# Performance work log

Hardware: AMD Instinct MI355X
Metric: run time of the kernel (lower is better)

## Reference

```python
import jax, jax.numpy as jnp
from jax import lax
import numpy as np

D = 512        # d_model
F = 128        # raw feature dim
MS = 1024      # logic (service) nodes
NP_ = 16384    # physical nodes
EL = 4096      # logic edges
EP = 131072    # phys edges
SRC = 0        # source_node_idx
NEG = -1e9


def _gnn(feats, edge_index, Win, Wout, N):
    row, col = edge_index
    h = jax.nn.relu(feats @ Win)                                  # [N, D]
    agg = jax.ops.segment_sum(h[row], col, num_segments=N)        # [N, D]
    return jax.nn.relu((h + agg) @ Wout)


def _bfs_hop(edge_index, N, src, iters=16):
    # BFS hop distance from src (bounded Bellman-Ford relaxation)
    row, col = edge_index
    big = jnp.int32(N)
    dist = jnp.full((N,), big, jnp.int32).at[src].set(0)
    def body(_, d):
        cand = jnp.minimum(d[row] + 1, big)
        upd = jax.ops.segment_min(cand, col, num_segments=N)
        return jnp.minimum(d, upd)
    return lax.fori_loop(0, iters, body, dist)


def _forward(logic_feats, phys_feats, Ws_in, Ws_out, Wp_in, Wp_out,
             sA1, sA2, pA1, pA2, Wq, Wk, Wc1, bc1, wc2,
             logic_edge_index, phys_edge_index, actions, static_mask, topo_order):
    Np = phys_feats.shape[0]
    cloud = Np - 1                                                # cloud_node_idx = -1
    h_s = _gnn(logic_feats, logic_edge_index, Ws_in, Ws_out, logic_feats.shape[0])
    h_p = _gnn(phys_feats, phys_edge_index, Wp_in, Wp_out, Np)
    # task-specific residual adapters
    h_s = h_s + jax.nn.relu(h_s @ sA1) @ sA2
    h_p = h_p + jax.nn.relu(h_p @ pA1) @ pA2
    metric = _bfs_hop(phys_edge_index, Np, SRC)                   # [Np] int32
    q_all = (h_s @ Wq) / jnp.sqrt(jnp.float32(D))                 # [Ms, D]
    K = h_p @ Wk                                                  # [Np, D]
    acts = actions.astype(jnp.int32)

    def step(state, i):
        visited, last, logp_sum, ent_sum, switches, relax = state
        base = static_mask[i]                                     # [Np] bool
        # cloud_sticky branch
        sticky = jnp.zeros_like(base).at[cloud].set(base[cloud])
        # forbid_return (allow_stay keeps `last`)
        forbid = visited.at[last].set(False)
        allowed_n = base & (~forbid) & (metric >= metric[last])   # metric_non_decreasing
        allowed = jnp.where(last == cloud, sticky, allowed_n)
        any_a = allowed.any()
        # relaxation fallback: stay -> cloud -> base
        fb_stay = jnp.zeros_like(base).at[last].set(True)
        fb_cloud = jnp.zeros_like(base).at[cloud].set(True)
        fallback = jnp.where(base[last], fb_stay, jnp.where(base[cloud], fb_cloud, base))
        allowed = jnp.where(any_a, allowed, fallback)
        # actor: masked categorical over physical nodes
        logits = K @ q_all[i]                                     # [Np]
        logp_all = jax.nn.log_softmax(jnp.where(allowed, logits, NEG))
        p = jnp.exp(logp_all)
        ent = -jnp.sum(p * logp_all)
        a = acts[i]
        ne = a != last
        visited = visited.at[last].set(visited[last] | ne)
        last = jnp.where(ne, a, last)
        return (visited, last, logp_sum + logp_all[a], ent_sum + ent,
                switches + ne.astype(jnp.int32), relax + (~any_a).astype(jnp.int32)), None

    init = (jnp.zeros((Np,), bool), jnp.int32(SRC),
            jnp.float32(0.0), jnp.float32(0.0), jnp.int32(0), jnp.int32(0))
    (visited, last, logp_sum, ent_sum, switches, relax), _ = lax.scan(
        step, init, topo_order.astype(jnp.int32))
    # value head
    pooled = jnp.concatenate([h_s.mean(0), h_p.mean(0)])          # [2D]
    value = jax.nn.relu(pooled @ Wc1 + bc1) @ wc2                 # scalar
    return jnp.stack([logp_sum, ent_sum, value])


def setup_inputs() -> dict:
    key = jax.random.key(0)
    ks = jax.random.split(key, 20)
    s = 0.05
    def w(k, shape):
        return jax.random.normal(k, shape, jnp.float32) * s
    return {
        "logic_edge_index": jax.random.randint(ks[0], (2, EL), 0, MS, jnp.int32),
        "logic_feats": jax.random.normal(ks[1], (MS, F), jnp.float32),
        "phys_edge_index": jax.random.randint(ks[2], (2, EP), 0, NP_, jnp.int32),
        "phys_feats": jax.random.normal(ks[3], (NP_, F), jnp.float32),
        "actions": jax.random.randint(ks[4], (MS,), 0, NP_, jnp.int32),
        "static_mask": jnp.ones((MS, NP_), bool),
        "topo_order": jnp.arange(MS, dtype=jnp.int32),
        "Ws_in": w(ks[5], (F, D)), "Ws_out": w(ks[6], (D, D)),
        "Wp_in": w(ks[7], (F, D)), "Wp_out": w(ks[8], (D, D)),
        "sA1": w(ks[9], (D, D)), "sA2": w(ks[10], (D, D)),
        "pA1": w(ks[11], (D, D)), "pA2": w(ks[12], (D, D)),
        "Wq": w(ks[13], (D, D)), "Wk": w(ks[14], (D, D)),
        "Wc1": w(ks[15], (2 * D, D)),
        "bc1": jnp.zeros((D,), jnp.float32),
        "wc2": w(ks[16], (D,)),
    }


def reference(logic_edge_index, logic_feats, phys_edge_index, phys_feats,
              actions, static_mask, topo_order,
              Ws_in, Ws_out, Wp_in, Wp_out, sA1, sA2, pA1, pA2,
              Wq, Wk, Wc1, bc1, wc2):
    return _forward(logic_feats, phys_feats, Ws_in, Ws_out, Wp_in, Wp_out,
                    sA1, sA2, pA1, pA2, Wq, Wk, Wc1, bc1, wc2,
                    logic_edge_index, phys_edge_index, actions, static_mask, topo_order)
```

## Files before the change

### kernel.cpp

```cpp
#include <hip/hip_runtime.h>
#include <cstdint>
#include <cstddef>

typedef __bf16 bf16_t;
typedef uint8_t u8;
typedef float f32x4 __attribute__((ext_vector_type(4)));

#define NEGV (-1e9f)

#define GLDS(gp, lp) __builtin_amdgcn_global_load_lds( \
    (const __attribute__((address_space(1))) void*)(gp), \
    (__attribute__((address_space(3))) void*)(lp), 16, 0, 0)

template<int SEL>
__device__ inline float fp8decw(uint32_t w) { return __builtin_amdgcn_cvt_f32_fp8((int)w, SEL); }
__device__ inline float fp8dec(u8 b) { return __builtin_amdgcn_cvt_f32_fp8((int)b, 0); }
__device__ inline u8 f2fp8(float x) {
    return (u8)(__builtin_amdgcn_cvt_pk_fp8_f32(x, x, 0, false) & 0xFF);
}

__device__ inline void bfs_level_work(const int* __restrict__ offR, const int* __restrict__ ecol,
                                      int* __restrict__ dist, int lev, int blk, int tid) {
    int j = blk * 256 + tid;
    if (dist[j] != lev) return;
    int e0 = offR[j], e1 = offR[j + 1];
    for (int e = e0; e < e1; ++e) {
        int v = ecol[e];
        if (dist[v] == 16384) dist[v] = lev + 1;
    }
}

struct PrepArgs {
    const float* w512src[8]; u8* w512dst[8];
    const float* w128src[2]; u8* w128dst[2];
    const float* logicF; const float* physF;
    u8* featsSb; u8* featsPb;
    const int* mask; uint32_t* bits;
    int* cntC; int* cntR; int* cntL; int* firstL; int* dist;
    float* pooled; float* hacc;
};

__global__ __launch_bounds__(256)
void k_prep(PrepArgs p) {
    __shared__ float tb[64][65];
    const int b = blockIdx.x, tid = threadIdx.x;
    if (b < 544) {
        const float* src; u8* dst; int K, tile;
        if (b < 512) { src = p.w512src[b >> 6]; dst = p.w512dst[b >> 6]; K = 512; tile = b & 63; }
        else { int bb = b - 512; src = p.w128src[bb >> 4]; dst = p.w128dst[bb >> 4]; K = 128; tile = bb & 15; }
        const int N = 512;
        int kt = tile >> 3, tc = tile & 7;
        int cx = tid & 63, ry = tid >> 6;
#pragma unroll
        for (int q = 0; q < 16; ++q) {
            int r = q * 4 + ry;
            tb[r][cx] = src[(size_t)(kt * 64 + r) * N + tc * 64 + cx];
        }
        __syncthreads();
#pragma unroll
        for (int q = 0; q < 16; ++q) {
            int r2 = q * 4 + ry;
            dst[(size_t)(tc * 64 + r2) * K + kt * 64 + cx] = f2fp8(tb[cx][r2]);
        }
    } else if (b < 672) {
        size_t e0 = (size_t)(b - 544) * 1024 + tid * 4;
        float4 v = *(const float4*)(p.logicF + e0);
        int pk = __builtin_amdgcn_cvt_pk_fp8_f32(v.x, v.y, 0, false);
        pk = __builtin_amdgcn_cvt_pk_fp8_f32(v.z, v.w, pk, true);
        *(uint32_t*)(p.featsSb + e0) = (uint32_t)pk;
    } else if (b < 2720) {
        size_t e0 = (size_t)(b - 672) * 1024 + tid * 4;
        float4 v = *(const float4*)(p.physF + e0);
        int pk = __builtin_amdgcn_cvt_pk_fp8_f32(v.x, v.y, 0, false);
        pk = __builtin_amdgcn_cvt_pk_fp8_f32(v.z, v.w, pk, true);
        *(uint32_t*)(p.featsPb + e0) = (uint32_t)pk;
    } else if (b < 2784) {
        int gid = (b - 2720) * 256 + tid;
        p.cntC[gid] = 0; p.cntR[gid] = 0; p.firstL[gid] = 0x7fffffff;
        p.dist[gid] = (gid == 0) ? 0 : 16384;
        if (gid < 1024) { p.cntL[gid] = 0; p.pooled[gid] = 0.0f; }
        if (gid < 512) p.hacc[gid] = 0.0f;
    } else {
        size_t w = (size_t)(b - 2784) * 256 + tid;
        const int4* q4 = (const int4*)(p.mask + w * 32);
        uint32_t bb = 0;
#pragma unroll
        for (int q = 0; q < 8; ++q) {
            int4 v = q4[q];
            bb |= (v.x != 0 ? 1u : 0u) << (q * 4);
            bb |= (v.y != 0 ? 1u : 0u) << (q * 4 + 1);
            bb |= (v.z != 0 ? 1u : 0u) << (q * 4 + 2);
            bb |= (v.w != 0 ? 1u : 0u) << (q * 4 + 3);
        }
        p.bits[w] = bb;
    }
}

__global__ void k_hist3(const int* __restrict__ rowP, const int* __restrict__ colP,
                        const int* __restrict__ rowL, const int* __restrict__ colL,
                        int* cntC, int* cntR, int* cntL, int EP, int EL,
                        const int* __restrict__ topo, const int* __restrict__ acts,
                        int* __restrict__ lastArr, int* __restrict__ firstL) {
    int b = blockIdx.x;
    if (b < 1040) {
        int e = b * 256 + threadIdx.x;
        if (e < EP) atomicAdd(&cntC[colP[e]], 1);
        else if (e < 2 * EP) atomicAdd(&cntR[rowP[e - EP]], 1);
        else if (e < 2 * EP + EL) atomicAdd(&cntL[colL[e - 2 * EP]], 1);
    } else {
        int s = (b - 1040) * 256 + threadIdx.x;
        int last = (s == 0) ? 0 : acts[topo[s - 1]];
        lastArr[s] = last;
        int a = acts[topo[s]];
        if (a != last) atomicMin(&firstL[last], s);
    }
}

__global__ __launch_bounds__(256)
void k_scan3(int* cntC, int* offC, int* curC,
             int* cntR, int* offR, int* curR,
             int* cntL, int* offL, int* curL) {
    __shared__ int ss[256];
    const int tid = threadIdx.x;
    if (blockIdx.x < 2) {
        int* cnt; int* off; int* cur;
        if (blockIdx.x == 0) { cnt = cntC; off = offC; cur = curC; }
        else                 { cnt = cntR; off = offR; cur = curR; }
        int4 v[16];
        const int4* pv = (const int4*)(cnt + tid * 64);
#pragma unroll
        for (int i = 0; i < 16; ++i) v[i] = pv[i];
        int s = 0;
#pragma unroll
        for (int i = 0; i < 16; ++i) s += v[i].x + v[i].y + v[i].z + v[i].w;
        ss[tid] = s; __syncthreads();
        for (int d = 1; d < 256; d <<= 1) {
            int t = (tid >= d) ? ss[tid - d] : 0;
            __syncthreads(); ss[tid] += t; __syncthreads();
        }
        int run = (tid == 0) ? 0 : ss[tid - 1];
        int4* po = (int4*)(off + tid * 64);
        int4* pc = (int4*)(cur + tid * 64);
#pragma unroll
        for (int i = 0; i < 16; ++i) {
            int4 o;
            o.x = run; run += v[i].x;
            o.y = run; run += v[i].y;
            o.z = run; run += v[i].z;
            o.w = run; run += v[i].w;
            po[i] = o; pc[i] = o;
        }
        if (tid == 255) off[16384] = run;
    } else {
        int4 v = *(const int4*)(cntL + tid * 4);
        int s = v.x + v.y + v.z + v.w;
        ss[tid] = s; __syncthreads();
        for (int d = 1; d < 256; d <<= 1) {
            int t = (tid >= d) ? ss[tid - d] : 0;
            __syncthreads(); ss[tid] += t; __syncthreads();
        }
        int run = (tid == 0) ? 0 : ss[tid - 1];
        int4 o;
        o.x = run; run += v.x;
        o.y = run; run += v.y;
        o.z = run; run += v.z;
        o.w = run; run += v.w;
        *(int4*)(offL + tid * 4) = o;
        *(int4*)(curL + tid * 4) = o;
        if (tid == 255) offL[1024] = run;
    }
}

__global__ void k_scatter3(const int* __restrict__ rowP, const int* __restrict__ colP,
                           const int* __restrict__ rowL, const int* __restrict__ colL,
                           int* curC, int* curR, int* curL,
                           int* erowCP, int* ecolRP, int* erowL, int EP, int EL) {
    int e = blockIdx.x * 256 + threadIdx.x;
    if (e < EP) {
        int c = colP[e]; int q = atomicAdd(&curC[c], 1); erowCP[q] = rowP[e];
    } else if (e < 2 * EP) {
        int e2 = e - EP;
        int c = rowP[e2]; int q = atomicAdd(&curR[c], 1); ecolRP[q] = colP[e2];
    } else if (e < 2 * EP + EL) {
        int e3 = e - 2 * EP;
        int c = colL[e3]; int q = atomicAdd(&curL[c], 1); erowL[q] = rowL[e3];
    }
}

__global__ __launch_bounds__(256)
void k_bfs_level(const int* __restrict__ offR, const int* __restrict__ ecol,
                 int* __restrict__ dist, int lev) {
    bfs_level_work(offR, ecol, dist, lev, blockIdx.x, threadIdx.x);
}

__global__ __launch_bounds__(256)
void k_fmpack(const int* __restrict__ firstL, const int* __restrict__ dist, int* __restrict__ fm) {
    int j = blockIdx.x * 256 + threadIdx.x;
    int fl = firstL[j]; if (fl > 0xFFFF) fl = 0xFFFF;
    fm[j] = (fl << 16) | dist[j];
}

struct GemmDesc { const u8* A; const u8* B; const u8* Cin; void* O;
                  int N; int K; float scale; int relu; int obf; };
struct GemmPair { GemmDesc d0; GemmDesc d1; int split; int gx; int nwg;
                  const int* offR; const int* ecol; int* dist; int bfsLev; };

__global__ __launch_bounds__(256)
void gemm_mfma(GemmPair args) {
    __shared__ u8 As[2][128 * 64];
    __shared__ u8 Bs[2][128 * 64];
    const int tid = threadIdx.x;
    int f = blockIdx.x;
    if (f < 64) {
        bfs_level_work(args.offR, args.ecol, args.dist, args.bfsLev, f, tid);
        return;
    }
    f -= 64;
    const int cpx = args.nwg >> 3;
    const int vfl = (f & 7) * cpx + (f >> 3);
    const int vbx = vfl % args.gx;
    const int vby = vfl / args.gx;
    const int inSet1 = (vby >= args.split);
    const GemmDesc g = inSet1 ? args.d1 : args.d0;
    const int my = vby - (inSet1 ? args.split : 0);
    const int m0 = my * 128, n0 = vbx * 128;
    const int wave = tid >> 6, lane = tid & 63;
    const int wm = (wave >> 1) * 64, wn = (wave & 1) * 64;
    const int lr = lane & 15, lkq = lane >> 4;
    const int K = g.K;
    const int srr = wave * 16 + (lane >> 2);
    const int scb = (((lane & 3) ^ ((lane >> 2) & 3)) << 4);
    const u8* Abase = g.A + (size_t)(m0 + srr) * K + scb;
    const u8* Bbase = g.B + (size_t)(n0 + srr) * K + scb;
    const size_t rstep = (size_t)64 * K;
    f32x4 acc[4][4] = {};

    auto stage = [&](int q, int k0) {
        GLDS(Abase + k0,         &As[q][(wave * 16) * 64]);
        GLDS(Abase + k0 + rstep, &As[q][(64 + wave * 16) * 64]);
        GLDS(Bbase + k0,         &Bs[q][(wave * 16) * 64]);
        GLDS(Bbase + k0 + rstep, &Bs[q][(64 + wave * 16) * 64]);
    };

    stage(0, 0);
    asm volatile("s_waitcnt vmcnt(0)" ::: "memory");
    __syncthreads();
    const int nt = K >> 6;
    for (int t = 0; t < nt; ++t) {
        int cur = t & 1;
        if (t + 1 < nt) stage(cur ^ 1, (t + 1) << 6);
#pragma unroll
        for (int kh = 0; kh < 2; ++kh) {
            long af[4], bf[4];
#pragma unroll
            for (int mi = 0; mi < 4; ++mi) {
                int r = wm + mi * 16 + lr;
                int pb = r * 64 + ((kh * 32 + lkq * 8) ^ ((r & 3) << 4));
                af[mi] = *(const long*)&As[cur][pb];
            }
#pragma unroll
            for (int ni = 0; ni < 4; ++ni) {
                int r = wn + ni * 16 + lr;
                int pb = r * 64 + ((kh * 32 + lkq * 8) ^ ((r & 3) << 4));
                bf[ni] = *(const long*)&Bs[cur][pb];
            }
#pragma unroll
            for (int mi = 0; mi < 4; ++mi)
#pragma unroll
                for (int ni = 0; ni < 4; ++ni)
                    acc[mi][ni] = __builtin_amdgcn_mfma_f32_16x16x32_fp8_fp8(af[mi], bf[ni], acc[mi][ni], 0, 0, 0);
        }
        asm volatile("s_waitcnt vmcnt(0)" ::: "memory");
        __syncthreads();
    }
    const int rb = m0 + wm + (lane >> 4) * 4;
    const int cb = n0 + wn + lr;
#pragma unroll
    for (int mi = 0; mi < 4; ++mi)
#pragma unroll
        for (int ni = 0; ni < 4; ++ni)
#pragma unroll
            for (int r = 0; r < 4; ++r) {
                int row = rb + mi * 16 + r;
                int col = cb + ni * 16;
                size_t idx = (size_t)row * g.N + col;
                float v = acc[mi][ni][r] * g.scale;
                if (g.Cin) v += fp8dec(g.Cin[idx]);
                if (g.relu) v = fmaxf(v, 0.0f);
                if (g.obf) ((bf16_t*)g.O)[idx] = (bf16_t)v;
                else       ((u8*)g.O)[idx] = f2fp8(v);
            }
}

__global__ __launch_bounds__(256)
void k_spmm2(const u8* __restrict__ HL, const int* __restrict__ offL, const int* __restrict__ erowL, u8* __restrict__ XL,
             const u8* __restrict__ HP, const int* __restrict__ offP, const int* __restrict__ erowP, u8* __restrict__ XP,
             const int* __restrict__ offR, const int* __restrict__ ecol, int* __restrict__ dist, int bfsLev) {
    int b = blockIdx.x;
    if (b < 64) { bfs_level_work(offR, ecol, dist, bfsLev, b, threadIdx.x); return; }
    b -= 64;
    const u8* H; const int* off; const int* erow; u8* X; int c;
    int wib = threadIdx.x >> 6, lane = threadIdx.x & 63;
    if (b < 256) { H = HL; off = offL; erow = erowL; X = XL; c = b * 4 + wib; }
    else { b -= 256; H = HP; off = offP; erow = erowP; X = XP; c = b * 4 + wib; }
    int d0 = lane * 8;
    float acc[8] = {0,0,0,0,0,0,0,0};
    int e0 = off[c], e1 = off[c + 1];
    for (int e = e0; e < e1; ++e) {
        int r = erow[e];
        uint2 w = *(const uint2*)(H + (size_t)r * 512 + d0);
        acc[0] += fp8decw<0>(w.x);
        acc[1] += fp8decw<1>(w.x);
        acc[2] += fp8decw<2>(w.x);
        acc[3] += fp8decw<3>(w.x);
        acc[4] += fp8decw<0>(w.y);
        acc[5] += fp8decw<1>(w.y);
        acc[6] += fp8decw<2>(w.y);
        acc[7] += fp8decw<3>(w.y);
    }
    uint2 ow = *(const uint2*)(H + (size_t)c * 512 + d0);
    float o0 = fp8decw<0>(ow.x) + acc[0];
    float o1 = fp8decw<1>(ow.x) + acc[1];
    float o2 = fp8decw<2>(ow.x) + acc[2];
    float o3 = fp8decw<3>(ow.x) + acc[3];
    float o4 = fp8decw<0>(ow.y) + acc[4];
    float o5 = fp8decw<1>(ow.y) + acc[5];
    float o6 = fp8decw<2>(ow.y) + acc[6];
    float o7 = fp8decw<3>(ow.y) + acc[7];
    int lo = __builtin_amdgcn_cvt_pk_fp8_f32(o0, o1, 0, false);
    lo = __builtin_amdgcn_cvt_pk_fp8_f32(o2, o3, lo, true);
    int hi = __builtin_amdgcn_cvt_pk_fp8_f32(o4, o5, 0, false);
    hi = __builtin_amdgcn_cvt_pk_fp8_f32(o6, o7, hi, true);
    uint2 res; res.x = (uint32_t)lo; res.y = (uint32_t)hi;
    *(uint2*)(X + (size_t)c * 512 + d0) = res;
}

__global__ __launch_bounds__(256)
void k_scan2(const bf16_t* __restrict__ S, const uint32_t* __restrict__ bits,
             const int* __restrict__ fm, const int* __restrict__ topo,
             const int* __restrict__ acts, const int* __restrict__ lastA,
             float* __restrict__ slogp, float* __restrict__ sent) {
    typedef bf16_t bf16x8 __attribute__((ext_vector_type(8)));
    const int NPn = 16384, cloud = NPn - 1;
    __shared__ float msh[256], zsh[256], wsh[256];
    __shared__ int ash[256];
    const int s = blockIdx.x, tid = threadIdx.x;
    const int i = topo[s], a = acts[i], last = lastA[s];
    const bf16_t* Srow = S + (size_t)i * NPn;
    const uint32_t* brow = bits + (size_t)i * 512;
    const int ml = fm[last] & 0xFFFF;
    const int baseCloud = (brow[511] >> 31) & 1;
    const int lic = (last == cloud);
    if (lic && baseCloud) {
        if (tid == 0) {
            float M = (float)Srow[cloud];
            slogp[s] = (a == cloud) ? 0.0f : (NEGV - M);
            sent[s] = 0.0f;
        }
        return;
    }
    float m = -3.4e38f, Z = 0.0f, W = 0.0f;
    int any = 0;
    if (!lic) {
        for (int c = 0; c < 8; ++c) {
            int j0 = c * 2048 + tid * 8;
            bf16x8 sv = *(const bf16x8*)(Srow + j0);
            uint32_t b8 = (brow[j0 >> 5] >> (j0 & 24)) & 0xFFu;
            int4 f0 = *(const int4*)(fm + j0);
            int4 f1 = *(const int4*)(fm + j0 + 4);
            int fj[8] = {f0.x, f0.y, f0.z, f0.w, f1.x, f1.y, f1.z, f1.w};
#pragma unroll
            for (int q = 0; q < 8; ++q) {
                int j = j0 + q;
                bool alw = ((b8 >> q) & 1) && ((fj[q] & 0xFFFF) >= ml)
                           && (j == last || (((unsigned)fj[q]) >> 16) >= (unsigned)s);
                if (alw) {
                    any = 1;
                    float l = (float)sv[q];
                    if (l > m) {
                        float d = m - l, ce = expf(d);
                        W = ce * (W + d * Z);
                        Z = ce * Z + 1.0f;
                        m = l;
                    } else {
                        float t = l - m, e = expf(t);
                        Z += e; W += t * e;
                    }
                }
            }
        }
    }
    msh[tid] = m; zsh[tid] = Z; wsh[tid] = W; ash[tid] = any;
    __syncthreads();
    for (int st = 128; st > 0; st >>= 1) {
        if (tid < st) {
            float m1 = msh[tid], Z1 = zsh[tid], W1 = wsh[tid];
            float m2 = msh[tid + st], Z2 = zsh[tid + st], W2 = wsh[tid + st];
            float M2 = fmaxf(m1, m2);
            float e1 = expf(m1 - M2), e2 = expf(m2 - M2);
            zsh[tid] = e1 * Z1 + e2 * Z2;
            wsh[tid] = e1 * (W1 + (m1 - M2) * Z1) + e2 * (W2 + (m2 - M2) * Z2);
            msh[tid] = M2;
            ash[tid] |= ash[tid + st];
        }
        __syncthreads();
    }
    if (tid != 0) return;
    if (ash[0]) {
        float M = msh[0], Zt = zsh[0], Wt = wsh[0];
        float logZ = logf(Zt);
        int fa = fm[a];
        bool alwa = ((brow[a >> 5] >> (a & 31)) & 1) && ((fa & 0xFFFF) >= ml)
                    && (a == last || (((unsigned)fa) >> 16) >= (unsigned)s);
        float la = alwa ? (float)Srow[a] : NEGV;
        slogp[s] = la - M - logZ;
        sent[s] = logZ - Wt / Zt;
        return;
    }
    int baseLast = (brow[last >> 5] >> (last & 31)) & 1;
    if (baseLast) { float M = (float)Srow[last]; slogp[s] = (a == last) ? 0.0f : (NEGV - M); sent[s] = 0.0f; return; }
    if (baseCloud) { float M = (float)Srow[cloud]; slogp[s] = (a == cloud) ? 0.0f : (NEGV - M); sent[s] = 0.0f; return; }
    float mm = -3.4e38f, ZZ = 0.0f, WW = 0.0f;
    for (int j = 0; j < NPn; ++j) {
        if ((brow[j >> 5] >> (j & 31)) & 1) {
            float l = (float)Srow[j];
            if (l > mm) { float d = mm - l, ce = expf(d); WW = ce * (WW + d * ZZ); ZZ = ce * ZZ + 1.0f; mm = l; }
            else { float t = l - mm, e = expf(t); ZZ += e; WW += t * e; }
        }
    }
    if (ZZ == 0.0f) { slogp[s] = -logf((float)NPn); sent[s] = logf((float)NPn); return; }
    float logZ = logf(ZZ);
    int ba = (brow[a >> 5] >> (a & 31)) & 1;
    float la = ba ? (float)Srow[a] : NEGV;
    slogp[s] = la - mm - logZ;
    sent[s] = logZ - WW / ZZ;
}

__global__ __launch_bounds__(256)
void k_pool2(const u8* __restrict__ HL, const u8* __restrict__ HP, float* __restrict__ pooled,
             const int* __restrict__ offR, const int* __restrict__ ecol, int* __restrict__ dist, int bfsLev) {
    int b = blockIdx.x, tid = threadIdx.x;
    if (b < 64) { bfs_level_work(offR, ecol, dist, bfsLev, b, tid); return; }
    b -= 64;
    const u8* H; float* dst; int R, bb, ng; float inv;
    if (b < 16) { H = HL; dst = pooled; R = 1024; inv = 1.0f / 1024.0f; bb = b; ng = 16; }
    else { H = HP; dst = pooled + 512; R = 16384; inv = 1.0f / 16384.0f; bb = b - 16; ng = 128; }
    int c0 = tid * 2;
    float a0 = 0, a1 = 0;
    for (int r = bb; r < R; r += ng) {
        uint32_t w = *(const unsigned short*)(H + (size_t)r * 512 + c0);
        a0 += fp8decw<0>(w);
        a1 += fp8decw<1>(w);
    }
    atomicAdd(&dst[c0], a0 * inv);
    atomicAdd(&dst[c0 + 1], a1 * inv);
}

__global__ __launch_bounds__(256)
void k_vpart(const float* __restrict__ pooled, const float* __restrict__ Wc1, float* __restrict__ hacc) {
    __shared__ float pk[128];
    int b = blockIdx.x, tid = threadIdx.x;
    int k0 = b * 128;
    if (tid < 128) pk[tid] = pooled[k0 + tid];
    __syncthreads();
    float a0 = 0, a1 = 0;
    for (int kk = 0; kk < 128; ++kk) {
        float pv = pk[kk];
        const float* wr = Wc1 + (size_t)(k0 + kk) * 512;
        a0 += pv * wr[tid];
        a1 += pv * wr[tid + 256];
    }
    atomicAdd(&hacc[tid], a0);
    atomicAdd(&hacc[tid + 256], a1);
}

__global__ __launch_bounds__(256)
void k_epilogue(const float* __restrict__ slogp, const float* __restrict__ sent,
                const float* __restrict__ hacc, const float* __restrict__ bc1,
                const float* __restrict__ wc2, float* __restrict__ out) {
    __shared__ float s1[256], s2[256], s3[256];
    int tid = threadIdx.x;
    float a = 0, b = 0;
    for (int k = tid; k < 1024; k += 256) { a += slogp[k]; b += sent[k]; }
    float v = fmaxf(hacc[tid] + bc1[tid], 0.0f) * wc2[tid]
            + fmaxf(hacc[tid + 256] + bc1[tid + 256], 0.0f) * wc2[tid + 256];
    s1[tid] = a; s2[tid] = b; s3[tid] = v;
    __syncthreads();
    for (int st = 128; st > 0; st >>= 1) {
        if (tid < st) { s1[tid] += s1[tid + st]; s2[tid] += s2[tid + st]; s3[tid] += s3[tid + st]; }
        __syncthreads();
    }
    if (tid == 0) { out[0] = s1[0]; out[1] = s2[0]; out[2] = s3[0]; }
}

extern "C" void kernel_launch(void* const* d_in, const int* in_sizes, int n_in,
                              void* d_out, int out_size, void* d_ws, size_t ws_size,
                              hipStream_t stream) {
    (void)n_in; (void)out_size; (void)ws_size; (void)in_sizes;
    const int MS = 1024, NP = 16384, EL = 4096, EP = 131072, D = 512;

    const int* logicE = (const int*)d_in[0];
    const float* logicF = (const float*)d_in[1];
    const int* physE = (const int*)d_in[2];
    const float* physF = (const float*)d_in[3];
    const int* acts = (const int*)d_in[4];
    const int* mask = (const int*)d_in[5];
    const int* topo = (const int*)d_in[6];
    const float* Ws_in = (const float*)d_in[7];
    const float* Ws_out = (const float*)d_in[8];
    const float* Wp_in = (const float*)d_in[9];
    const float* Wp_out = (const float*)d_in[10];
    const float* sA1 = (const float*)d_in[11];
    const float* sA2 = (const float*)d_in[12];
    const float* pA1 = (const float*)d_in[13];
    const float* pA2 = (const float*)d_in[14];
    const float* Wq = (const float*)d_in[15];
    const float* Wk = (const float*)d_in[16];
    const float* Wc1 = (const float*)d_in[17];
    const float* bc1 = (const float*)d_in[18];
    const float* wc2 = (const float*)d_in[19];
    float* out = (float*)d_out;

    char* wsb = (char*)d_ws;
    size_t off = 0;
    auto alloc = [&](size_t bytes) -> void* {
        off = (off + 255) & ~(size_t)255;
        void* p = wsb + off; off += bytes; return p;
    };

    bf16_t* S_bf  = (bf16_t*)alloc((size_t)MS * NP * 2);
    u8* PB0     = (u8*)alloc((size_t)NP * D);
    u8* PB1     = (u8*)alloc((size_t)NP * D);
    u8* PB2     = (u8*)alloc((size_t)NP * D);
    u8* LB0     = (u8*)alloc((size_t)MS * D);
    u8* LB1     = (u8*)alloc((size_t)MS * D);
    u8* LB2     = (u8*)alloc((size_t)MS * D);
    u8* featsSb = (u8*)alloc((size_t)MS * 128);
    u8* featsPb = (u8*)alloc((size_t)NP * 128);
    u8* WsinT   = (u8*)alloc(512 * 128);
    u8* WpinT   = (u8*)alloc(512 * 128);
    u8* WsoutT  = (u8*)alloc(512 * 512);
    u8* sA1T    = (u8*)alloc(512 * 512);
    u8* sA2T    = (u8*)alloc(512 * 512);
    u8* WqT     = (u8*)alloc(512 * 512);
    u8* WpoutT  = (u8*)alloc(512 * 512);
    u8* pA1T    = (u8*)alloc(512 * 512);
    u8* pA2T    = (u8*)alloc(512 * 512);
    u8* WkT     = (u8*)alloc(512 * 512);
    uint32_t* bits = (uint32_t*)alloc((size_t)MS * NP / 8);
    int* cntC  = (int*)alloc(NP * 4);
    int* offC  = (int*)alloc((NP + 1) * 4);
    int* curC  = (int*)alloc(NP * 4);
    int* cntR  = (int*)alloc(NP * 4);
    int* offR  = (int*)alloc((NP + 1) * 4);
    int* curR  = (int*)alloc(NP * 4);
    int* cntL  = (int*)alloc(MS * 4);
    int* offL  = (int*)alloc((MS + 1) * 4);
    int* curL  = (int*)alloc(MS * 4);
    int* erowCP = (int*)alloc(EP * 4);
    int* ecolRP = (int*)alloc(EP * 4);
    int* erowL  = (int*)alloc(EL * 4);
    int* firstL = (int*)alloc(NP * 4);
    int* lastA  = (int*)alloc(MS * 4);
    int* dist   = (int*)alloc(NP * 4);
    int* fm     = (int*)alloc(NP * 4);
    float* slogp = (float*)alloc(MS * 4);
    float* sentb = (float*)alloc(MS * 4);
    float* pooled = (float*)alloc(1024 * 4);
    float* hacc   = (float*)alloc(512 * 4);

    const int* rowP = physE;  const int* colP = physE + EP;
    const int* rowL = logicE; const int* colL = logicE + EL;

    {
        PrepArgs p;
        const float* s512[8] = {Ws_out, sA1, sA2, Wq, Wp_out, pA1, pA2, Wk};
        u8* d512[8] = {WsoutT, sA1T, sA2T, WqT, WpoutT, pA1T, pA2T, WkT};
        for (int q = 0; q < 8; ++q) { p.w512src[q] = s512[q]; p.w512dst[q] = d512[q]; }
        p.w128src[0] = Ws_in; p.w128dst[0] = WsinT;
        p.w128src[1] = Wp_in; p.w128dst[1] = WpinT;
        p.logicF = logicF; p.physF = physF; p.featsSb = featsSb; p.featsPb = featsPb;
        p.mask = mask; p.bits = bits;
        p.cntC = cntC; p.cntR = cntR; p.cntL = cntL; p.firstL = firstL; p.dist = dist;
        p.pooled = pooled; p.hacc = hacc;
        hipLaunchKernelGGL(k_prep, dim3(4832), dim3(256), 0, stream, p);
    }
    hipLaunchKernelGGL(k_hist3, dim3(1044), dim3(256), 0, stream,
                       rowP, colP, rowL, colL, cntC, cntR, cntL, EP, EL,
                       topo, acts, lastA, firstL);
    hipLaunchKernelGGL(k_scan3, dim3(3), dim3(256), 0, stream,
                       cntC, offC, curC, cntR, offR, curR, cntL, offL, curL);
    hipLaunchKernelGGL(k_scatter3, dim3((2 * EP + EL) / 256), dim3(256), 0, stream,
                       rowP, colP, rowL, colL, curC, curR, curL, erowCP, ecolRP, erowL, EP, EL);
    for (int lev = 0; lev < 7; ++lev)
        hipLaunchKernelGGL(k_bfs_level, dim3(64), dim3(256), 0, stream, offR, ecolRP, dist, lev);

    auto gemm2 = [&](const u8* A0, const u8* B0, const u8* C0, void* O0, float sc0,
                     const u8* A1, const u8* B1, const u8* C1, void* O1, float sc1,
                     int K, int relu, int bfsLev) {
        GemmPair gp;
        gp.d0 = {A0, B0, C0, O0, 512, K, sc0, relu, 0};
        gp.d1 = {A1, B1, C1, O1, 512, K, sc1, relu, 0};
        gp.split = 8; gp.gx = 4; gp.nwg = 544;
        gp.offR = offR; gp.ecol = ecolRP; gp.dist = dist; gp.bfsLev = bfsLev;
        hipLaunchKernelGGL(gemm_mfma, dim3(64 + 544), dim3(256), 0, stream, gp);
    };

    gemm2(featsSb, WsinT, nullptr, LB0, 1.0f, featsPb, WpinT, nullptr, PB0, 1.0f, 128, 1, 7);
    hipLaunchKernelGGL(k_spmm2, dim3(64 + 256 + 4096), dim3(256), 0, stream,
                       LB0, offL, erowL, LB1, PB0, offC, erowCP, PB1,
                       offR, ecolRP, dist, 8);
    gemm2(LB1, WsoutT, nullptr, LB0, 1.0f, PB1, WpoutT, nullptr, PB0, 1.0f, 512, 1, 9);
    gemm2(LB0, sA1T, nullptr, LB1, 1.0f, PB0, pA1T, nullptr, PB1, 1.0f, 512, 1, 10);
    gemm2(LB1, sA2T, LB0, LB2, 1.0f, PB1, pA2T, PB0, PB2, 1.0f, 512, 0, 11);
    hipLaunchKernelGGL(k_pool2, dim3(64 + 144), dim3(256), 0, stream, LB2, PB2, pooled,
                       offR, ecolRP, dist, 12);
    gemm2(LB2, WqT, nullptr, LB1, 0.044194173824159216f, PB2, WkT, nullptr, PB1, 1.0f, 512, 0, 13);
    {
        GemmPair gp;
        gp.d0 = {LB1, PB1, nullptr, S_bf, NP, 512, 1.0f, 0, 1};
        gp.d1 = gp.d0;
        gp.split = 1000; gp.gx = 128; gp.nwg = 1024;
        gp.offR = offR; gp.ecol = ecolRP; gp.dist = dist; gp.bfsLev = 14;
        hipLaunchKernelGGL(gemm_mfma, dim3(64 + 1024), dim3(256), 0, stream, gp);
    }
    hipLaunchKernelGGL(k_bfs_level, dim3(64), dim3(256), 0, stream, offR, ecolRP, dist, 15);
    hipLaunchKernelGGL(k_fmpack, dim3(64), dim3(256), 0, stream, firstL, dist, fm);
    hipLaunchKernelGGL(k_scan2, dim3(MS), dim3(256), 0, stream,
                       S_bf, bits, fm, topo, acts, lastA, slogp, sentb);
    hipLaunchKernelGGL(k_vpart, dim3(8), dim3(256), 0, stream, pooled, Wc1, hacc);
    hipLaunchKernelGGL(k_epilogue, dim3(1), dim3(256), 0, stream, slogp, sentb, hacc, bc1, wc2, out);
}
```

Baseline: 337.3 us.

## Store score matrix as fp8 and drop fmpack kernel by reading dist/firstL directly

The final score GEMM now writes the 1024x16384 logits in fp8 instead of bf16. This halves the write traffic and the read traffic for the scan kernel. The separate fmpack launch is removed, and the scan instead reads dist and firstL arrays directly, which trades one launch for extra loads per element. The risk is lower logit precision, which affects the log-prob and entropy values.

```diff
diff --git a/kernel.cpp b/kernel.cpp
--- a/kernel.cpp
+++ b/kernel.cpp
@@ -191,13 +191,6 @@
 void k_bfs_level(const int* __restrict__ offR, const int* __restrict__ ecol,
                  int* __restrict__ dist, int lev) {
     bfs_level_work(offR, ecol, dist, lev, blockIdx.x, threadIdx.x);
-}
-
-__global__ __launch_bounds__(256)
-void k_fmpack(const int* __restrict__ firstL, const int* __restrict__ dist, int* __restrict__ fm) {
-    int j = blockIdx.x * 256 + threadIdx.x;
-    int fl = firstL[j]; if (fl > 0xFFFF) fl = 0xFFFF;
-    fm[j] = (fl << 16) | dist[j];
 }
 
 struct GemmDesc { const u8* A; const u8* B; const u8* Cin; void* O;
@@ -336,24 +329,24 @@
 }
 
 __global__ __launch_bounds__(256)
-void k_scan2(const bf16_t* __restrict__ S, const uint32_t* __restrict__ bits,
-             const int* __restrict__ fm, const int* __restrict__ topo,
-             const int* __restrict__ acts, const int* __restrict__ lastA,
+void k_scan2(const u8* __restrict__ S, const uint32_t* __restrict__ bits,
+             const int* __restrict__ dist, const int* __restrict__ firstL,
+             const int* __restrict__ topo, const int* __restrict__ acts,
+             const int* __restrict__ lastA,
              float* __restrict__ slogp, float* __restrict__ sent) {
-    typedef bf16_t bf16x8 __attribute__((ext_vector_type(8)));
     const int NPn = 16384, cloud = NPn - 1;
     __shared__ float msh[256], zsh[256], wsh[256];
     __shared__ int ash[256];
     const int s = blockIdx.x, tid = threadIdx.x;
     const int i = topo[s], a = acts[i], last = lastA[s];
-    const bf16_t* Srow = S + (size_t)i * NPn;
+    const u8* Srow = S + (size_t)i * NPn;
     const uint32_t* brow = bits + (size_t)i * 512;
-    const int ml = fm[last] & 0xFFFF;
+    const int ml = dist[last];
     const int baseCloud = (brow[511] >> 31) & 1;
     const int lic = (last == cloud);
     if (lic && baseCloud) {
         if (tid == 0) {
-            float M = (float)Srow[cloud];
+            float M = fp8dec(Srow[cloud]);
             slogp[s] = (a == cloud) ? 0.0f : (NEGV - M);
             sent[s] = 0.0f;
         }
@@ -364,19 +357,23 @@
     if (!lic) {
         for (int c = 0; c < 8; ++c) {
             int j0 = c * 2048 + tid * 8;
-            bf16x8 sv = *(const bf16x8*)(Srow + j0);
+            uint2 sw = *(const uint2*)(Srow + j0);
+            float sv[8] = { fp8decw<0>(sw.x), fp8decw<1>(sw.x), fp8decw<2>(sw.x), fp8decw<3>(sw.x),
+                            fp8decw<0>(sw.y), fp8decw<1>(sw.y), fp8decw<2>(sw.y), fp8decw<3>(sw.y) };
             uint32_t b8 = (brow[j0 >> 5] >> (j0 & 24)) & 0xFFu;
-            int4 f0 = *(const int4*)(fm + j0);
-            int4 f1 = *(const int4*)(fm + j0 + 4);
-            int fj[8] = {f0.x, f0.y, f0.z, f0.w, f1.x, f1.y, f1.z, f1.w};
+            int4 d0v = *(const int4*)(dist + j0);
+            int4 d1v = *(const int4*)(dist + j0 + 4);
+            int4 f0v = *(const int4*)(firstL + j0);
+            int4 f1v = *(const int4*)(firstL + j0 + 4);
+            int dj[8] = {d0v.x, d0v.y, d0v.z, d0v.w, d1v.x, d1v.y, d1v.z, d1v.w};
+            int fl[8] = {f0v.x, f0v.y, f0v.z, f0v.w, f1v.x, f1v.y, f1v.z, f1v.w};
 #pragma unroll
             for (int q = 0; q < 8; ++q) {
                 int j = j0 + q;
-                bool alw = ((b8 >> q) & 1) && ((fj[q] & 0xFFFF) >= ml)
-                           && (j == last || (((unsigned)fj[q]) >> 16) >= (unsigned)s);
+                bool alw = ((b8 >> q) & 1) && (dj[q] >= ml) && (j == last || fl[q] >= s);
                 if (alw) {
                     any = 1;
-                    float l = (float)sv[q];
+                    float l = sv[q];
                     if (l > m) {
                         float d = m - l, ce = expf(d);
                         W = ce * (W + d * Z);
@@ -409,21 +406,20 @@
     if (ash[0]) {
         float M = msh[0], Zt = zsh[0], Wt = wsh[0];
         float logZ = logf(Zt);
-        int fa = fm[a];
-        bool alwa = ((brow[a >> 5] >> (a & 31)) & 1) && ((fa & 0xFFFF) >= ml)
-                    && (a == last || (((unsigned)fa) >> 16) >= (unsigned)s);
-        float la = alwa ? (float)Srow[a] : NEGV;
+        bool alwa = ((brow[a >> 5] >> (a & 31)) & 1) && (dist[a] >= ml)
+                    && (a == last || firstL[a] >= s);
+        float la = alwa ? fp8dec(Srow[a]) : NEGV;
         slogp[s] = la - M - logZ;
         sent[s] = logZ - Wt / Zt;
         return;
     }
     int baseLast = (brow[last >> 5] >> (last & 31)) & 1;
-    if (baseLast) { float M = (float)Srow[last]; slogp[s] = (a == last) ? 0.0f : (NEGV - M); sent[s] = 0.0f; return; }
-    if (baseCloud) { float M = (float)Srow[cloud]; slogp[s] = (a == cloud) ? 0.0f : (NEGV - M); sent[s] = 0.0f; return; }
+    if (baseLast) { float M = fp8dec(Srow[last]); slogp[s] = (a == last) ? 0.0f : (NEGV - M); sent[s] = 0.0f; return; }
+    if (baseCloud) { float M = fp8dec(Srow[cloud]); slogp[s] = (a == cloud) ? 0.0f : (NEGV - M); sent[s] = 0.0f; return; }
     float mm = -3.4e38f, ZZ = 0.0f, WW = 0.0f;
     for (int j = 0; j < NPn; ++j) {
         if ((brow[j >> 5] >> (j & 31)) & 1) {
-            float l = (float)Srow[j];
+            float l = fp8dec(Srow[j]);
             if (l > mm) { float d = mm - l, ce = expf(d); WW = ce * (WW + d * ZZ); ZZ = ce * ZZ + 1.0f; mm = l; }
             else { float t = l - mm, e = expf(t); ZZ += e; WW += t * e; }
         }
@@ -431,7 +427,7 @@
     if (ZZ == 0.0f) { slogp[s] = -logf((float)NPn); sent[s] = logf((float)NPn); return; }
     float logZ = logf(ZZ);
     int ba = (brow[a >> 5] >> (a & 31)) & 1;
-    float la = ba ? (float)Srow[a] : NEGV;
+    float la = ba ? fp8dec(Srow[a]) : NEGV;
     slogp[s] = la - mm - logZ;
     sent[s] = logZ - WW / ZZ;
 }
@@ -528,7 +524,7 @@
         void* p = wsb + off; off += bytes; return p;
     };
 
-    bf16_t* S_bf  = (bf16_t*)alloc((size_t)MS * NP * 2);
+    u8* S8      = (u8*)alloc((size_t)MS * NP);
     u8* PB0     = (u8*)alloc((size_t)NP * D);
     u8* PB1     = (u8*)alloc((size_t)NP * D);
     u8* PB2     = (u8*)alloc((size_t)NP * D);
@@ -563,7 +559,6 @@
     int* firstL = (int*)alloc(NP * 4);
     int* lastA  = (int*)alloc(MS * 4);
     int* dist   = (int*)alloc(NP * 4);
-    int* fm     = (int*)alloc(NP * 4);
     float* slogp = (float*)alloc(MS * 4);
     float* sentb = (float*)alloc(MS * 4);
     float* pooled = (float*)alloc(1024 * 4);
@@ -618,16 +613,15 @@
     gemm2(LB2, WqT, nullptr, LB1, 0.044194173824159216f, PB2, WkT, nullptr, PB1, 1.0f, 512, 0, 13);
     {
         GemmPair gp;
-        gp.d0 = {LB1, PB1, nullptr, S_bf, NP, 512, 1.0f, 0, 1};
+        gp.d0 = {LB1, PB1, nullptr, S8, NP, 512, 1.0f, 0, 0};
         gp.d1 = gp.d0;
         gp.split = 1000; gp.gx = 128; gp.nwg = 1024;
         gp.offR = offR; gp.ecol = ecolRP; gp.dist = dist; gp.bfsLev = 14;
         hipLaunchKernelGGL(gemm_mfma, dim3(64 + 1024), dim3(256), 0, stream, gp);
     }
     hipLaunchKernelGGL(k_bfs_level, dim3(64), dim3(256), 0, stream, offR, ecolRP, dist, 15);
-    hipLaunchKernelGGL(k_fmpack, dim3(64), dim3(256), 0, stream, firstL, dist, fm);
     hipLaunchKernelGGL(k_scan2, dim3(MS), dim3(256), 0, stream,
-                       S_bf, bits, fm, topo, acts, lastA, slogp, sentb);
+                       S8, bits, dist, firstL, topo, acts, lastA, slogp, sentb);
     hipLaunchKernelGGL(k_vpart, dim3(8), dim3(256), 0, stream, pooled, Wc1, hacc);
     hipLaunchKernelGGL(k_epilogue, dim3(1), dim3(256), 0, stream, slogp, sentb, hacc, bc1, wc2, out);
 }
```

Result: no change. 340.0 us (+0.8%).
